# Kernel optimization log

Hardware: AMD Instinct MI355X
Metric: run time of the kernel (lower is better)

## Reference

```python
import jax, jax.numpy as jnp
import numpy as np
from jax.ops import segment_sum

N = 100000      # nodes
E = 1600000     # edges
G = 128         # graphs in batch
D = 128         # input (embedding) dim
H = 128         # hidden dim
WALK = 16       # random-walk length
PED = 16        # PE embed dim
L = 5           # GNN layers
OUT = 10        # classes
EPS = 1e-5      # batchnorm eps


def setup_inputs() -> dict:
    key = jax.random.key(0)
    ks = jax.random.split(key, 32)
    f = lambda k, shp: (jax.random.normal(k, shp, dtype=jnp.float32) * 0.05)
    inp = {
        'x': jnp.zeros((N,), dtype=jnp.int64) if jax.config.jax_enable_x64 else jnp.zeros((N,), dtype=jnp.int32),
        'edge_index': jax.random.randint(ks[0], (2, E), 0, N),
        'batch': jnp.sort(jax.random.randint(ks[1], (N,), 0, G)),
        'emb_table': f(ks[2], (1, D)),
        'pe_w': f(ks[3], (WALK, PED)), 'pe_b': f(ks[4], (PED,)),
        'proj_w': f(ks[5], (D + PED, H)), 'proj_b': f(ks[6], (H,)),
        'gin_w1': f(ks[7], (L, H, H)), 'gin_b1': f(ks[8], (L, H)),
        'gin_w2': f(ks[9], (L, H, H)), 'gin_b2': f(ks[10], (L, H)),
        'bn_g': jnp.ones((L, H), jnp.float32), 'bn_b': jnp.zeros((L, H), jnp.float32),
        'ffn_w1': f(ks[11], (L, H, 2 * H)), 'ffn_b1': f(ks[12], (L, 2 * H)),
        'ffn_w2': f(ks[13], (L, 2 * H, H)), 'ffn_b2': f(ks[14], (L, H)),
        'ffn_bn_g': jnp.ones((L, H), jnp.float32), 'ffn_bn_b': jnp.zeros((L, H), jnp.float32),
        'out_w1': f(ks[15], (H, H)), 'out_b1': f(ks[16], (H,)),
        'out_w2': f(ks[17], (H, OUT)), 'out_b2': f(ks[18], (OUT,)),
    }
    return inp


def _batchnorm(h, g, b):
    # BatchNorm1d forward with batch statistics (training-mode math)
    mu = jnp.mean(h, axis=0)
    var = jnp.var(h, axis=0)
    return (h - mu) * jax.lax.rsqrt(var + EPS) * g + b


def _forward(emb_table, pe_w, pe_b, proj_w, proj_b, gin_w1, gin_b1, gin_w2, gin_b2,
             bn_g, bn_b, ffn_w1, ffn_b1, ffn_w2, ffn_b2, ffn_bn_g, ffn_bn_b,
             out_w1, out_b1, out_w2, out_b2, x, edge_index, batch):
    h0 = emb_table[x]                                # [N, D] (all indices are 0)

    # ---- RandomWalkPositionalEncoding (vectorized scatter-add per step) ----
    row0, col0 = edge_index[0], edge_index[1]
    loops = jnp.arange(N)
    row = jnp.concatenate([row0, loops])
    col = jnp.concatenate([col0, loops])             # self loops appended
    deg = segment_sum(jnp.ones(row.shape, jnp.float32), col, num_segments=N)
    dinv = jnp.where(deg > 0, jax.lax.rsqrt(jnp.maximum(deg, 1.0)), 0.0)
    norm_e = dinv[row] * dinv[col]                   # [E+N]

    cnt = segment_sum(jnp.ones((N,), jnp.float32), batch, num_segments=G)
    prob = 1.0 / jnp.maximum(cnt, 1.0)[batch]        # per-graph uniform init

    def rw_step(p, _):
        new_p = segment_sum(p[row] * norm_e, col, num_segments=N)
        return new_p * 0.9 + p * 0.1, p

    _, rw = jax.lax.scan(rw_step, prob, None, length=WALK)   # [WALK, N]
    pe = rw.T @ pe_w + pe_b                          # [N, PED]

    # ---- input projection ----
    h = jnp.concatenate([h0, pe], axis=-1) @ proj_w + proj_b # [N, H]

    # ---- stacked GIN layers with BN, residual and FFN (dropout = eval identity) ----
    for i in range(L):
        res = h
        agg = segment_sum(h[row0], col0, num_segments=N) + h  # GIN: (1+eps)x + sum_j x_j, eps=0
        z = jax.nn.relu(agg @ gin_w1[i] + gin_b1[i]) @ gin_w2[i] + gin_b2[i]
        z = jax.nn.relu(_batchnorm(z, bn_g[i], bn_b[i]))
        h = z + res
        res2 = h
        f = jax.nn.relu(h @ ffn_w1[i] + ffn_b1[i]) @ ffn_w2[i] + ffn_b2[i]
        h = _batchnorm(f + res2, ffn_bn_g[i], ffn_bn_b[i])

    # ---- global mean pooling + MLP head ----
    gsum = segment_sum(h, batch, num_segments=G)
    g = gsum / jnp.maximum(cnt, 1.0)[:, None]        # [G, H]
    out = jax.nn.relu(g @ out_w1 + out_b1) @ out_w2 + out_b2
    return out                                        # [G, OUT]


def reference(x, edge_index, batch, emb_table, pe_w, pe_b, proj_w, proj_b,
              gin_w1, gin_b1, gin_w2, gin_b2, bn_g, bn_b, ffn_w1, ffn_b1,
              ffn_w2, ffn_b2, ffn_bn_g, ffn_bn_b, out_w1, out_b1, out_w2, out_b2):
    return _forward(emb_table, pe_w, pe_b, proj_w, proj_b, gin_w1, gin_b1, gin_w2,
                    gin_b2, bn_g, bn_b, ffn_w1, ffn_b1, ffn_w2, ffn_b2,
                    ffn_bn_g, ffn_bn_b, out_w1, out_b1, out_w2, out_b2,
                    x, edge_index, batch)
```

## Files before the change

### kernel.cpp

```cpp
#include <hip/hip_runtime.h>
#include <math.h>

#define NN 100000
#define NE 1600000
#define NG 128
#define HD 128
#define WLK 16
#define NL 5
#define NOUT 10
#define BNEPS 1e-5f
#define CDIV(a,b) (((a)+(b)-1)/(b))

#define NBKT 782
#define NEB 400
#define EPB 4000
#define NSCAN (NBKT*NEB)
#define NSB CDIV(NSCAN,1024)
#define NBM 782

typedef float f32x4 __attribute__((ext_vector_type(4)));
typedef _Float16 f16x8 __attribute__((ext_vector_type(8)));
typedef unsigned short ushort_t;
typedef unsigned int uint_t;

__device__ __forceinline__ ushort_t f2h(float x) {
    union { _Float16 h; ushort_t u; } c;
    c.h = (_Float16)x;
    return c.u;
}
__device__ __forceinline__ float h2f(ushort_t u) {
    union { ushort_t u; _Float16 h; } c;
    c.u = u;
    return (float)c.h;
}

__global__ void k_cnt(const int* __restrict__ batch, int* __restrict__ cnt,
                      int* __restrict__ goff) {
    int g = threadIdx.x;
    if (g >= NG) return;
    int lo0 = 0, hi0 = NN;
    while (lo0 < hi0) { int m = (lo0 + hi0) >> 1; if (batch[m] < g) lo0 = m + 1; else hi0 = m; }
    int lo1 = lo0, hi1 = NN;
    while (lo1 < hi1) { int m = (lo1 + hi1) >> 1; if (batch[m] < g + 1) lo1 = m + 1; else hi1 = m; }
    cnt[g] = lo1 - lo0;
    goff[g] = lo0;
}

__global__ void k_bhist(const int* __restrict__ col0, int* __restrict__ bhist) {
    __shared__ int hist[NBKT];
    for (int i = threadIdx.x; i < NBKT; i += 256) hist[i] = 0;
    __syncthreads();
    int e0 = blockIdx.x * EPB;
    for (int e = e0 + threadIdx.x; e < e0 + EPB; e += 256) atomicAdd(&hist[col0[e] >> 7], 1);
    __syncthreads();
    for (int i = threadIdx.x; i < NBKT; i += 256) bhist[i * NEB + blockIdx.x] = hist[i];
}

__global__ void k_gscan1(const int* __restrict__ in, int* __restrict__ bsum) {
    __shared__ int sm[256];
    int base = blockIdx.x * 1024 + threadIdx.x * 4;
    int s = 0;
#pragma unroll
    for (int i = 0; i < 4; ++i) { int e = base + i; if (e < NSCAN) s += in[e]; }
    sm[threadIdx.x] = s; __syncthreads();
    for (int st = 128; st > 0; st >>= 1) {
        if (threadIdx.x < st) sm[threadIdx.x] += sm[threadIdx.x + st];
        __syncthreads();
    }
    if (threadIdx.x == 0) bsum[blockIdx.x] = sm[0];
}

__global__ void k_scan2(int* __restrict__ blksum, int nblk) {
    __shared__ int sm[512];
    int t = threadIdx.x;
    int x = (t < nblk) ? blksum[t] : 0;
    sm[t] = x; __syncthreads();
    for (int s = 1; s < 512; s <<= 1) {
        int v = (t >= s) ? sm[t - s] : 0;
        __syncthreads();
        sm[t] += v;
        __syncthreads();
    }
    if (t < nblk) blksum[t] = sm[t] - x;
}

__global__ void k_gscan3(const int* __restrict__ in, const int* __restrict__ bsum,
                         int* __restrict__ out) {
    __shared__ int sm[256];
    int t = threadIdx.x;
    int base = blockIdx.x * 1024 + t * 4;
    int v[4]; int s = 0;
#pragma unroll
    for (int i = 0; i < 4; ++i) { int e = base + i; v[i] = (e < NSCAN) ? in[e] : 0; s += v[i]; }
    sm[t] = s; __syncthreads();
    for (int st = 1; st < 256; st <<= 1) {
        int x = (t >= st) ? sm[t - st] : 0;
        __syncthreads();
        sm[t] += x;
        __syncthreads();
    }
    int excl = sm[t] - s + bsum[blockIdx.x];
#pragma unroll
    for (int i = 0; i < 4; ++i) { int e = base + i; if (e < NSCAN) { out[e] = excl; excl += v[i]; } }
}

__global__ void k_escatter(const int* __restrict__ row0, const int* __restrict__ col0,
                           const int* __restrict__ boffs, int2* __restrict__ epair) {
    __shared__ int cur[NBKT];
    for (int i = threadIdx.x; i < NBKT; i += 256) cur[i] = boffs[i * NEB + blockIdx.x];
    __syncthreads();
    int e0 = blockIdx.x * EPB;
    for (int e = e0 + threadIdx.x; e < e0 + EPB; e += 256) {
        int c = col0[e], r = row0[e];
        int pos = atomicAdd(&cur[c >> 7], 1);
        epair[pos] = make_int2(c, r);
    }
}

__global__ void k_bucket(const int2* __restrict__ epair, const int* __restrict__ boffs,
                         int* __restrict__ rowptr, int* __restrict__ deg,
                         int* __restrict__ esrc) {
    __shared__ int cnt_[128], scn[128], cur_[128];
    int bkt = blockIdx.x, t = threadIdx.x;
    int bs = boffs[bkt * NEB];
    int be = (bkt + 1 < NBKT) ? boffs[(bkt + 1) * NEB] : NE;
    if (t < 128) cnt_[t] = 0;
    __syncthreads();
    for (int e = bs + t; e < be; e += 256) atomicAdd(&cnt_[epair[e].x & 127], 1);
    __syncthreads();
    int c = (t < 128) ? cnt_[t] : 0;
    if (t < 128) scn[t] = c;
    __syncthreads();
    for (int st = 1; st < 128; st <<= 1) {
        int x = (t >= st && t < 128) ? scn[t - st] : 0;
        __syncthreads();
        if (t < 128) scn[t] += x;
        __syncthreads();
    }
    if (t < 128) {
        int excl = scn[t] - c;
        int node = bkt * 128 + t;
        if (node < NN) { rowptr[node] = bs + excl; deg[node] = c; }
        cur_[t] = bs + excl;
    }
    if (bkt == NBKT - 1 && t == 0) rowptr[NN] = NE;
    __syncthreads();
    for (int e = bs + t; e < be; e += 256) {
        int2 p = epair[e];
        int pos = atomicAdd(&cur_[p.x & 127], 1);
        esrc[pos] = p.y;
    }
}

__global__ void k_init_pe(const int* __restrict__ deg, const int* __restrict__ batch,
                          const int* __restrict__ cnt, float* __restrict__ dinv,
                          float* __restrict__ p, float* __restrict__ pd) {
    int v = blockIdx.x * 256 + threadIdx.x;
    if (v >= NN) return;
    float dv = rsqrtf((float)(deg[v] + 1));
    dinv[v] = dv;
    float pv = 1.0f / fmaxf((float)cnt[batch[v]], 1.0f);
    p[v] = pv; pd[v] = pv * dv;
}

__global__ void k_rw_step(const float* __restrict__ pin, const float* __restrict__ pdin,
                          const int* __restrict__ rowptr, const int* __restrict__ esrc,
                          const float* __restrict__ dinv, float* __restrict__ rwslice,
                          float* __restrict__ pout, float* __restrict__ pdout) {
    int v = blockIdx.x * 256 + threadIdx.x;
    if (v >= NN) return;
    int b = rowptr[v], e = rowptr[v + 1];
    float a0 = 0.f, a1 = 0.f, a2 = 0.f, a3 = 0.f;
    int i = b;
    for (; i + 4 <= e; i += 4) {
        int s0 = esrc[i], s1 = esrc[i + 1], s2 = esrc[i + 2], s3 = esrc[i + 3];
        a0 += pdin[s0]; a1 += pdin[s1]; a2 += pdin[s2]; a3 += pdin[s3];
    }
    for (; i < e; ++i) a0 += pdin[esrc[i]];
    float s = (a0 + a1) + (a2 + a3);
    float dv = dinv[v];
    float pv = pin[v];
    float np = s * dv + pv * dv * dv;
    float nxt = 0.9f * np + 0.1f * pv;
    rwslice[v] = pv;
    pout[v] = nxt;
    pdout[v] = nxt * dv;
}

__global__ void k_mc1(const float* __restrict__ emb, const float* __restrict__ pe_w,
                      const float* __restrict__ pe_b, const float* __restrict__ proj_w,
                      const float* __restrict__ proj_b, float* __restrict__ M,
                      float* __restrict__ c1) {
    int j = threadIdx.x;
    float c0 = proj_b[j];
    for (int d = 0; d < HD; ++d) c0 += emb[d] * proj_w[d * HD + j];
    for (int w = 0; w < WLK; ++w) c0 += pe_b[w] * proj_w[(HD + w) * HD + j];
    c1[j] = c0;
    for (int s = 0; s < WLK; ++s) {
        float m = 0.f;
        for (int w = 0; w < WLK; ++w) m += pe_w[s * WLK + w] * proj_w[(HD + w) * HD + j];
        M[s * HD + j] = m;
    }
}

__global__ void k_proj(const float* __restrict__ rw, const float* __restrict__ M,
                       const float* __restrict__ c1, float4* __restrict__ h4,
                       uint2* __restrict__ hb4) {
    int idx = blockIdx.x * 256 + threadIdx.x;
    if (idx >= NN * 32) return;
    int v = idx >> 5, cg = (idx & 31) * 4;
    float4 acc = *(const float4*)&c1[cg];
#pragma unroll
    for (int s = 0; s < WLK; ++s) {
        float r = rw[s * NN + v];
        float4 m = *(const float4*)&M[s * HD + cg];
        acc.x += r * m.x; acc.y += r * m.y; acc.z += r * m.z; acc.w += r * m.w;
    }
    h4[idx] = acc;
    hb4[idx] = make_uint2((uint_t)f2h(acc.x) | ((uint_t)f2h(acc.y) << 16),
                          (uint_t)f2h(acc.z) | ((uint_t)f2h(acc.w) << 16));
}

__global__ void k_prepw(const float* __restrict__ g1, const float* __restrict__ g2,
                        const float* __restrict__ f1, const float* __restrict__ f2,
                        ushort_t* __restrict__ wt1, ushort_t* __restrict__ wt2,
                        ushort_t* __restrict__ wt3, ushort_t* __restrict__ wt4) {
    int i = blockIdx.x * 256 + threadIdx.x;
    if (i < 81920) {
        int l = i >> 14, rem = i & 16383, n = rem >> 7, k = rem & 127;
        wt1[i] = f2h(g1[l * 16384 + k * 128 + n]);
    } else if (i < 163840) {
        int j = i - 81920;
        int l = j >> 14, rem = j & 16383, n = rem >> 7, k = rem & 127;
        wt2[j] = f2h(g2[l * 16384 + k * 128 + n]);
    } else if (i < 327680) {
        int j = i - 163840;
        int l = j >> 15, rem = j & 32767, n = rem >> 7, k = rem & 127;
        wt3[j] = f2h(f1[l * 32768 + k * 256 + n]);
    } else {
        int j = i - 327680;
        int l = j >> 15, rem = j & 32767, n = rem >> 8, k = rem & 255;
        wt4[j] = f2h(f2[l * 32768 + k * 128 + n]);
    }
}

__global__ void k_aggb(const uint_t* __restrict__ hb2, const int* __restrict__ rowptr,
                       const int* __restrict__ esrc, uint_t* __restrict__ aggb2) {
    int wave = threadIdx.x >> 6, lane = threadIdx.x & 63;
    int v = blockIdx.x * 4 + wave;
    if (v >= NN) return;
    uint_t u = hb2[(size_t)v * 64 + lane];
    float sx[8], sy[8];
#pragma unroll
    for (int k = 0; k < 8; ++k) { sx[k] = 0.f; sy[k] = 0.f; }
    sx[0] = h2f((ushort_t)(u & 0xFFFFu)); sy[0] = h2f((ushort_t)(u >> 16));
    int b = rowptr[v], e = rowptr[v + 1];
    int i = b;
    for (; i + 8 <= e; i += 8) {
        int idx[8]; uint_t x[8];
#pragma unroll
        for (int k = 0; k < 8; ++k) idx[k] = esrc[i + k];
#pragma unroll
        for (int k = 0; k < 8; ++k) x[k] = hb2[(size_t)idx[k] * 64 + lane];
#pragma unroll
        for (int k = 0; k < 8; ++k) {
            sx[k] += h2f((ushort_t)(x[k] & 0xFFFFu));
            sy[k] += h2f((ushort_t)(x[k] >> 16));
        }
    }
    for (; i < e; ++i) {
        uint_t x = hb2[(size_t)esrc[i] * 64 + lane];
        sx[0] += h2f((ushort_t)(x & 0xFFFFu)); sy[0] += h2f((ushort_t)(x >> 16));
    }
    float fx = ((sx[0] + sx[1]) + (sx[2] + sx[3])) + ((sx[4] + sx[5]) + (sx[6] + sx[7]));
    float fy = ((sy[0] + sy[1]) + (sy[2] + sy[3])) + ((sy[4] + sy[5]) + (sy[6] + sy[7]));
    aggb2[(size_t)v * 64 + lane] = (uint_t)f2h(fx) | ((uint_t)f2h(fy) << 16);
}

#define GLDK 136
__global__ __launch_bounds__(256)
void k_gin(const ushort_t* __restrict__ A, const ushort_t* __restrict__ W1T,
           const ushort_t* __restrict__ W2T, const float* __restrict__ b1,
           const float* __restrict__ b2, ushort_t* __restrict__ z2h,
           float* __restrict__ partS, float* __restrict__ partQ) {
    __shared__ ushort_t As[128 * GLDK];
    __shared__ ushort_t Ws[64 * GLDK];
    __shared__ float sS[128], sQ[128];
    const int tid = threadIdx.x;
    const int w = tid >> 6, l = tid & 63;
    const int lm = l & 15, lq = l >> 4;
    const int rw0 = w * 32;
    const int vr0 = blockIdx.x * 128;
    if (tid < 128) { sS[tid] = 0.f; sQ[tid] = 0.f; }

#pragma unroll
    for (int it = 0; it < 8; ++it) {
        int f = it * 256 + tid;
        int row = f >> 4, sl = f & 15;
        uint4 a = make_uint4(0, 0, 0, 0);
        int vr = vr0 + row;
        if (vr < NN) a = *(const uint4*)&A[(size_t)vr * HD + sl * 8];
        *(uint4*)&As[row * GLDK + sl * 8] = a;
    }

    f32x4 z1a[2][2][4] = {};
    for (int c = 0; c < 2; ++c) {
        __syncthreads();
#pragma unroll
        for (int it = 0; it < 4; ++it) {
            int f = it * 256 + tid;
            int row = f >> 4, sl = f & 15;
            *(uint4*)&Ws[row * GLDK + sl * 8] =
                *(const uint4*)&W1T[(size_t)(c * 64 + row) * HD + sl * 8];
        }
        __syncthreads();
#pragma unroll
        for (int kk = 0; kk < 128; kk += 32) {
            f16x8 af[2], bf[4];
#pragma unroll
            for (int i = 0; i < 2; ++i)
                af[i] = *(const f16x8*)&As[(rw0 + i * 16 + lm) * GLDK + kk + lq * 8];
#pragma unroll
            for (int j = 0; j < 4; ++j)
                bf[j] = *(const f16x8*)&Ws[(j * 16 + lm) * GLDK + kk + lq * 8];
#pragma unroll
            for (int i = 0; i < 2; ++i)
#pragma unroll
                for (int j = 0; j < 4; ++j)
                    z1a[c][i][j] = __builtin_amdgcn_mfma_f32_16x16x32_f16(af[i], bf[j], z1a[c][i][j], 0, 0, 0);
        }
    }
    __syncthreads();

#pragma unroll
    for (int c = 0; c < 2; ++c)
#pragma unroll
        for (int j = 0; j < 4; ++j) {
            int col = c * 64 + j * 16 + lm;
            float bj = b1[col];
#pragma unroll
            for (int i = 0; i < 2; ++i)
#pragma unroll
                for (int r = 0; r < 4; ++r) {
                    int row = rw0 + i * 16 + lq * 4 + r;
                    As[row * GLDK + col] = f2h(fmaxf(z1a[c][i][j][r] + bj, 0.f));
                }
        }

    f32x4 z2a[2][2][4] = {};
    for (int c2 = 0; c2 < 2; ++c2) {
        __syncthreads();
#pragma unroll
        for (int it = 0; it < 4; ++it) {
            int f = it * 256 + tid;
            int row = f >> 4, sl = f & 15;
            *(uint4*)&Ws[row * GLDK + sl * 8] =
                *(const uint4*)&W2T[(size_t)(c2 * 64 + row) * HD + sl * 8];
        }
        __syncthreads();
#pragma unroll
        for (int kk = 0; kk < 128; kk += 32) {
            f16x8 af[2], bf[4];
#pragma unroll
            for (int i = 0; i < 2; ++i)
                af[i] = *(const f16x8*)&As[(rw0 + i * 16 + lm) * GLDK + kk + lq * 8];
#pragma unroll
            for (int j = 0; j < 4; ++j)
                bf[j] = *(const f16x8*)&Ws[(j * 16 + lm) * GLDK + kk + lq * 8];
#pragma unroll
            for (int i = 0; i < 2; ++i)
#pragma unroll
                for (int j = 0; j < 4; ++j)
                    z2a[c2][i][j] = __builtin_amdgcn_mfma_f32_16x16x32_f16(af[i], bf[j], z2a[c2][i][j], 0, 0, 0);
        }
    }

    float ls[2][4] = {}, lsq[2][4] = {};
#pragma unroll
    for (int c2 = 0; c2 < 2; ++c2)
#pragma unroll
        for (int j = 0; j < 4; ++j) {
            int col = c2 * 64 + j * 16 + lm;
            float bj = b2[col];
#pragma unroll
            for (int i = 0; i < 2; ++i)
#pragma unroll
                for (int r = 0; r < 4; ++r) {
                    int vr = vr0 + rw0 + i * 16 + lq * 4 + r;
                    if (vr < NN) {
                        float x = z2a[c2][i][j][r] + bj;
                        ls[c2][j] += x; lsq[c2][j] += x * x;
                        z2h[(size_t)vr * HD + col] = f2h(x);
                    }
                }
        }
#pragma unroll
    for (int c2 = 0; c2 < 2; ++c2)
#pragma unroll
        for (int j = 0; j < 4; ++j) {
            atomicAdd(&sS[c2 * 64 + j * 16 + lm], ls[c2][j]);
            atomicAdd(&sQ[c2 * 64 + j * 16 + lm], lsq[c2][j]);
        }
    __syncthreads();
    if (tid < 128) {
        partS[(size_t)tid * NBM + blockIdx.x] = sS[tid];
        partQ[(size_t)tid * NBM + blockIdx.x] = sQ[tid];
    }
}

template <int K, bool RELU, bool OUTH16, bool ADDRES, bool DOSTATS>
__global__ __launch_bounds__(256, 2)
void k_mgemm(const ushort_t* __restrict__ A, const ushort_t* __restrict__ WT,
             const float* __restrict__ bias, ushort_t* __restrict__ Ch,
             float* __restrict__ Cf, const float* __restrict__ res,
             float* __restrict__ partS, float* __restrict__ partQ, int ncols) {
    constexpr int LDK = 72;
    __shared__ ushort_t As[128 * LDK];
    __shared__ ushort_t Ws[128 * LDK];
    __shared__ float sS[128], sQ[128];
    const int tid = threadIdx.x;
    const int w = tid >> 6, l = tid & 63;
    const int lm = l & 15, lq = l >> 4;
    const int rb = (w >> 1) * 64, cbw = (w & 1) * 64;
    const int vr0 = blockIdx.x * 128;
    const int cb = blockIdx.y * 128;
    f32x4 acc[4][4] = {};

    for (int kt = 0; kt < K / 64; ++kt) {
        __syncthreads();
#pragma unroll
        for (int it = 0; it < 4; ++it) {
            int f = it * 256 + tid;
            int row = f >> 3, sl = f & 7;
            uint4 a = make_uint4(0, 0, 0, 0);
            int vr = vr0 + row;
            if (vr < NN) a = *(const uint4*)&A[(size_t)vr * K + kt * 64 + sl * 8];
            *(uint4*)&As[row * LDK + sl * 8] = a;
            uint4 wv = *(const uint4*)&WT[(size_t)(cb + row) * K + kt * 64 + sl * 8];
            *(uint4*)&Ws[row * LDK + sl * 8] = wv;
        }
        __syncthreads();
#pragma unroll
        for (int kk = 0; kk < 64; kk += 32) {
            f16x8 af[4], bf[4];
#pragma unroll
            for (int i = 0; i < 4; ++i)
                af[i] = *(const f16x8*)&As[(rb + i * 16 + lm) * LDK + kk + lq * 8];
#pragma unroll
            for (int j = 0; j < 4; ++j)
                bf[j] = *(const f16x8*)&Ws[(cbw + j * 16 + lm) * LDK + kk + lq * 8];
#pragma unroll
            for (int i = 0; i < 4; ++i)
#pragma unroll
                for (int j = 0; j < 4; ++j)
                    acc[i][j] = __builtin_amdgcn_mfma_f32_16x16x32_f16(af[i], bf[j], acc[i][j], 0, 0, 0);
        }
    }

    float bcol[4];
#pragma unroll
    for (int j = 0; j < 4; ++j) bcol[j] = bias[cb + cbw + j * 16 + lm];
    if (DOSTATS && tid < 128) { sS[tid] = 0.f; sQ[tid] = 0.f; }
    __syncthreads();
    float ls[4] = {0, 0, 0, 0}, lsq[4] = {0, 0, 0, 0};
#pragma unroll
    for (int i = 0; i < 4; ++i) {
#pragma unroll
        for (int r = 0; r < 4; ++r) {
            int vr = vr0 + rb + i * 16 + lq * 4 + r;
            if (vr < NN) {
#pragma unroll
                for (int j = 0; j < 4; ++j) {
                    float x = acc[i][j][r] + bcol[j];
                    if (RELU) x = fmaxf(x, 0.f);
                    int c = cb + cbw + j * 16 + lm;
                    if (ADDRES) x += res[(size_t)vr * ncols + c];
                    if (DOSTATS) { ls[j] += x; lsq[j] += x * x; }
                    if (OUTH16) Ch[(size_t)vr * ncols + c] = f2h(x);
                    else        Cf[(size_t)vr * ncols + c] = x;
                }
            }
        }
    }
    if (DOSTATS) {
#pragma unroll
        for (int j = 0; j < 4; ++j) {
            atomicAdd(&sS[cbw + j * 16 + lm], ls[j]);
            atomicAdd(&sQ[cbw + j * 16 + lm], lsq[j]);
        }
        __syncthreads();
        if (tid < 128) {
            partS[(size_t)(cb + tid) * NBM + blockIdx.x] = sS[tid];
            partQ[(size_t)(cb + tid) * NBM + blockIdx.x] = sQ[tid];
        }
    }
}

__global__ void k_bnparm(const float* __restrict__ partS, const float* __restrict__ partQ,
                         const float* __restrict__ g, const float* __restrict__ b,
                         float* __restrict__ bnA, float* __restrict__ bnB) {
    __shared__ float smS[256], smQ[256];
    int c = blockIdx.x, t = threadIdx.x;
    float s = 0.f, q = 0.f;
    for (int i = t; i < NBM; i += 256) {
        s += partS[(size_t)c * NBM + i];
        q += partQ[(size_t)c * NBM + i];
    }
    smS[t] = s; smQ[t] = q; __syncthreads();
    for (int st = 128; st > 0; st >>= 1) {
        if (t < st) { smS[t] += smS[t + st]; smQ[t] += smQ[t + st]; }
        __syncthreads();
    }
    if (t == 0) {
        float mu = smS[0] * (1.0f / NN);
        float var = smQ[0] * (1.0f / NN) - mu * mu;
        float inv = rsqrtf(var + BNEPS);
        float a = g[c] * inv;
        bnA[c] = a;
        bnB[c] = b[c] - mu * a;
    }
}

__global__ void k_bn_relu_res(const uint2* __restrict__ z4, const float* __restrict__ bnA,
                              const float* __restrict__ bnB, float4* __restrict__ h4,
                              uint2* __restrict__ hb4) {
    int idx = blockIdx.x * 256 + threadIdx.x;
    if (idx >= NN * 32) return;
    int cg = (idx & 31) * 4;
    float4 A = *(const float4*)&bnA[cg];
    float4 B = *(const float4*)&bnB[cg];
    uint2 zv = z4[idx];
    float z0 = h2f((ushort_t)(zv.x & 0xFFFFu)), z1 = h2f((ushort_t)(zv.x >> 16));
    float z2 = h2f((ushort_t)(zv.y & 0xFFFFu)), z3 = h2f((ushort_t)(zv.y >> 16));
    float4 hv = h4[idx];
    float4 nh;
    nh.x = hv.x + fmaxf(z0 * A.x + B.x, 0.f);
    nh.y = hv.y + fmaxf(z1 * A.y + B.y, 0.f);
    nh.z = hv.z + fmaxf(z2 * A.z + B.z, 0.f);
    nh.w = hv.w + fmaxf(z3 * A.w + B.w, 0.f);
    h4[idx] = nh;
    hb4[idx] = make_uint2((uint_t)f2h(nh.x) | ((uint_t)f2h(nh.y) << 16),
                          (uint_t)f2h(nh.z) | ((uint_t)f2h(nh.w) << 16));
}

__global__ void k_bn(const uint2* __restrict__ t4, const float* __restrict__ bnA,
                     const float* __restrict__ bnB, float4* __restrict__ h4,
                     uint2* __restrict__ hb4) {
    int idx = blockIdx.x * 256 + threadIdx.x;
    if (idx >= NN * 32) return;
    int cg = (idx & 31) * 4;
    float4 A = *(const float4*)&bnA[cg];
    float4 B = *(const float4*)&bnB[cg];
    uint2 tv = t4[idx];
    float t0 = h2f((ushort_t)(tv.x & 0xFFFFu)), t1 = h2f((ushort_t)(tv.x >> 16));
    float t2 = h2f((ushort_t)(tv.y & 0xFFFFu)), t3 = h2f((ushort_t)(tv.y >> 16));
    float4 nh;
    nh.x = t0 * A.x + B.x;
    nh.y = t1 * A.y + B.y;
    nh.z = t2 * A.z + B.z;
    nh.w = t3 * A.w + B.w;
    h4[idx] = nh;
    hb4[idx] = make_uint2((uint_t)f2h(nh.x) | ((uint_t)f2h(nh.y) << 16),
                          (uint_t)f2h(nh.z) | ((uint_t)f2h(nh.w) << 16));
}

__global__ void k_pool(const float4* __restrict__ h4, const int* __restrict__ goff,
                       const int* __restrict__ cnt, float* __restrict__ gsum) {
    __shared__ float4 sm[256];
    int g = blockIdx.x >> 2, sub = blockIdx.x & 3;
    int n0 = goff[g], n = cnt[g];
    int cg = threadIdx.x & 31, rl = threadIdx.x >> 5;
    float4 acc = make_float4(0.f, 0.f, 0.f, 0.f);
    for (int r = sub * 8 + rl; r < n; r += 32) {
        float4 v = h4[(size_t)(n0 + r) * 32 + cg];
        acc.x += v.x; acc.y += v.y; acc.z += v.z; acc.w += v.w;
    }
    sm[threadIdx.x] = acc; __syncthreads();
    for (int st = 128; st >= 32; st >>= 1) {
        if (threadIdx.x < st) {
            float4 o = sm[threadIdx.x + st];
            sm[threadIdx.x].x += o.x; sm[threadIdx.x].y += o.y;
            sm[threadIdx.x].z += o.z; sm[threadIdx.x].w += o.w;
        }
        __syncthreads();
    }
    if (threadIdx.x < 32) {
        float4 v = sm[threadIdx.x];
        atomicAdd(&gsum[g * HD + cg * 4 + 0], v.x);
        atomicAdd(&gsum[g * HD + cg * 4 + 1], v.y);
        atomicAdd(&gsum[g * HD + cg * 4 + 2], v.z);
        atomicAdd(&gsum[g * HD + cg * 4 + 3], v.w);
    }
}

__global__ void k_head(const float* __restrict__ gsum, const int* __restrict__ cnt,
                       const float* __restrict__ w1, const float* __restrict__ b1,
                       const float* __restrict__ w2, const float* __restrict__ b2,
                       float* __restrict__ out) {
    __shared__ float gv[HD], av[HD];
    int gid = blockIdx.x, t = threadIdx.x;
    float c = fmaxf((float)cnt[gid], 1.0f);
    gv[t] = gsum[gid * HD + t] / c;
    __syncthreads();
    float a = b1[t];
    for (int k = 0; k < HD; ++k) a += gv[k] * w1[k * HD + t];
    av[t] = fmaxf(a, 0.f);
    __syncthreads();
    if (t < NOUT) {
        float o = b2[t];
        for (int k = 0; k < HD; ++k) o += av[k] * w2[k * NOUT + t];
        out[gid * NOUT + t] = o;
    }
}

static constexpr size_t AL(size_t x) { return (x + 511) & ~(size_t)511; }
static constexpr size_t OFF_H      = 0;
static constexpr size_t OFF_HB     = OFF_H      + AL((size_t)NN * HD * 4);
static constexpr size_t OFF_BUFF   = OFF_HB     + AL((size_t)NN * HD * 2);
static constexpr size_t OFF_SHARE  = OFF_BUFF   + AL((size_t)NN * HD * 4);
static constexpr size_t SZ_SHARE   = AL((size_t)NN * 256 * 2);
static constexpr size_t OFF_RW     = OFF_SHARE  + SZ_SHARE;
static constexpr size_t OFF_P0     = OFF_RW     + AL((size_t)WLK * NN * 4);
static constexpr size_t OFF_P1     = OFF_P0     + AL((size_t)NN * 4);
static constexpr size_t OFF_PD0    = OFF_P1     + AL((size_t)NN * 4);
static constexpr size_t OFF_PD1    = OFF_PD0    + AL((size_t)NN * 4);
static constexpr size_t OFF_DINV   = OFF_PD1    + AL((size_t)NN * 4);
static constexpr size_t OFF_ESRC   = OFF_DINV   + AL((size_t)NN * 4);
static constexpr size_t OFF_ROWPTR = OFF_ESRC   + AL((size_t)NE * 4);
static constexpr size_t OFF_DEG    = OFF_ROWPTR + AL((size_t)(NN + 1) * 4);
static constexpr size_t OFF_BHIST  = OFF_DEG    + AL((size_t)NN * 4);
static constexpr size_t OFF_BOFFS  = OFF_BHIST  + AL((size_t)NSCAN * 4);
static constexpr size_t OFF_BSUM   = OFF_BOFFS  + AL((size_t)NSCAN * 4);
static constexpr size_t OFF_WT1    = OFF_BSUM   + AL(512 * 4);
static constexpr size_t OFF_WT2    = OFF_WT1    + AL((size_t)5 * 16384 * 2);
static constexpr size_t OFF_WT3    = OFF_WT2    + AL((size_t)5 * 16384 * 2);
static constexpr size_t OFF_WT4    = OFF_WT3    + AL((size_t)5 * 32768 * 2);
static constexpr size_t OFF_PARTS  = OFF_WT4    + AL((size_t)5 * 32768 * 2);
static constexpr size_t OFF_PARTQ  = OFF_PARTS  + AL((size_t)128 * NBM * 4);
static constexpr size_t OFF_BNA    = OFF_PARTQ  + AL((size_t)128 * NBM * 4);
static constexpr size_t OFF_BNB    = OFF_BNA    + AL(128 * 4);
static constexpr size_t OFF_M      = OFF_BNB    + AL(128 * 4);
static constexpr size_t OFF_C1     = OFF_M      + AL((size_t)WLK * HD * 4);
static constexpr size_t OFF_CNT    = OFF_C1     + AL(HD * 4);
static constexpr size_t OFF_GOFF   = OFF_CNT    + AL(NG * 4);
static constexpr size_t OFF_GSUM   = OFF_GOFF   + AL(NG * 4);
static constexpr size_t ZERO_BYTES = (size_t)NG * HD * 4;

extern "C" void kernel_launch(void* const* d_in, const int* in_sizes, int n_in,
                              void* d_out, int out_size, void* d_ws, size_t ws_size,
                              hipStream_t stream) {
    const int* eidx = (const int*)d_in[1];
    const int* row0 = eidx;
    const int* col0 = eidx + NE;
    const int* batch = (const int*)d_in[2];
    const float* emb = (const float*)d_in[3];
    const float* pe_w = (const float*)d_in[4];
    const float* pe_b = (const float*)d_in[5];
    const float* proj_w = (const float*)d_in[6];
    const float* proj_b = (const float*)d_in[7];
    const float* gin_w1 = (const float*)d_in[8];
    const float* gin_b1 = (const float*)d_in[9];
    const float* gin_w2 = (const float*)d_in[10];
    const float* gin_b2 = (const float*)d_in[11];
    const float* bn_g = (const float*)d_in[12];
    const float* bn_b = (const float*)d_in[13];
    const float* ffn_w1 = (const float*)d_in[14];
    const float* ffn_b1 = (const float*)d_in[15];
    const float* ffn_w2 = (const float*)d_in[16];
    const float* ffn_b2 = (const float*)d_in[17];
    const float* ffn_bn_g = (const float*)d_in[18];
    const float* ffn_bn_b = (const float*)d_in[19];
    const float* out_w1 = (const float*)d_in[20];
    const float* out_b1 = (const float*)d_in[21];
    const float* out_w2 = (const float*)d_in[22];
    const float* out_b2 = (const float*)d_in[23];
    float* out = (float*)d_out;

    char* ws = (char*)d_ws;
    float*    h     = (float*)(ws + OFF_H);
    ushort_t* hb    = (ushort_t*)(ws + OFF_HB);
    ushort_t* th    = (ushort_t*)(ws + OFF_BUFF);
    ushort_t* aggh  = (ushort_t*)(ws + OFF_SHARE);
    ushort_t* z2h   = (ushort_t*)(ws + OFF_SHARE + (size_t)NN * HD * 2);
    ushort_t* f1h   = (ushort_t*)(ws + OFF_SHARE);
    int2*     epair = (int2*)(ws + OFF_SHARE);
    float*    rw    = (float*)(ws + OFF_RW);
    float*    p0    = (float*)(ws + OFF_P0);
    float*    p1    = (float*)(ws + OFF_P1);
    float*    pd0   = (float*)(ws + OFF_PD0);
    float*    pd1   = (float*)(ws + OFF_PD1);
    float*    dinv  = (float*)(ws + OFF_DINV);
    int*      esrc  = (int*)(ws + OFF_ESRC);
    int*      rowptr= (int*)(ws + OFF_ROWPTR);
    int*      deg   = (int*)(ws + OFF_DEG);
    int*      bhist = (int*)(ws + OFF_BHIST);
    int*      boffs = (int*)(ws + OFF_BOFFS);
    int*      bsum  = (int*)(ws + OFF_BSUM);
    ushort_t* wt1   = (ushort_t*)(ws + OFF_WT1);
    ushort_t* wt2   = (ushort_t*)(ws + OFF_WT2);
    ushort_t* wt3   = (ushort_t*)(ws + OFF_WT3);
    ushort_t* wt4   = (ushort_t*)(ws + OFF_WT4);
    float*    partS = (float*)(ws + OFF_PARTS);
    float*    partQ = (float*)(ws + OFF_PARTQ);
    float*    bnA   = (float*)(ws + OFF_BNA);
    float*    bnB   = (float*)(ws + OFF_BNB);
    float*    M     = (float*)(ws + OFF_M);
    float*    c1    = (float*)(ws + OFF_C1);
    int*      cnt   = (int*)(ws + OFF_CNT);
    int*      goff  = (int*)(ws + OFF_GOFF);
    float*    gsum  = (float*)(ws + OFF_GSUM);

    const int NB = CDIV(NN, 256);
    const int NBV = CDIV(NN * 32, 256);

    hipMemsetAsync(ws + OFF_GSUM, 0, ZERO_BYTES, stream);

    k_cnt<<<1, 128, 0, stream>>>(batch, cnt, goff);
    k_bhist<<<NEB, 256, 0, stream>>>(col0, bhist);
    k_gscan1<<<NSB, 256, 0, stream>>>(bhist, bsum);
    k_scan2<<<1, 512, 0, stream>>>(bsum, NSB);
    k_gscan3<<<NSB, 256, 0, stream>>>(bhist, bsum, boffs);
    k_escatter<<<NEB, 256, 0, stream>>>(row0, col0, boffs, epair);
    k_bucket<<<NBKT, 256, 0, stream>>>(epair, boffs, rowptr, deg, esrc);

    k_init_pe<<<NB, 256, 0, stream>>>(deg, batch, cnt, dinv, p0, pd0);
    k_mc1<<<1, 128, 0, stream>>>(emb, pe_w, pe_b, proj_w, proj_b, M, c1);
    k_prepw<<<1920, 256, 0, stream>>>(gin_w1, gin_w2, ffn_w1, ffn_w2, wt1, wt2, wt3, wt4);
    for (int s = 0; s < WLK; ++s) {
        const float* pin = (s & 1) ? p1 : p0;
        const float* pdin = (s & 1) ? pd1 : pd0;
        float* pout = (s & 1) ? p0 : p1;
        float* pdout = (s & 1) ? pd0 : pd1;
        k_rw_step<<<NB, 256, 0, stream>>>(pin, pdin, rowptr, esrc, dinv,
                                          rw + (size_t)s * NN, pout, pdout);
    }
    k_proj<<<NBV, 256, 0, stream>>>(rw, M, c1, (float4*)h, (uint2*)hb);

    dim3 g1(NBM, 1), g2(NBM, 2);
    for (int i = 0; i < NL; ++i) {
        k_aggb<<<CDIV(NN, 4), 256, 0, stream>>>((const uint_t*)hb, rowptr, esrc, (uint_t*)aggh);
        k_gin<<<NBM, 256, 0, stream>>>(aggh, wt1 + (size_t)i * 16384, wt2 + (size_t)i * 16384,
                                       gin_b1 + i * HD, gin_b2 + i * HD, z2h, partS, partQ);
        k_bnparm<<<128, 256, 0, stream>>>(partS, partQ, bn_g + i * HD, bn_b + i * HD, bnA, bnB);
        k_bn_relu_res<<<NBV, 256, 0, stream>>>(
            (const uint2*)z2h, bnA, bnB, (float4*)h, (uint2*)hb);
        k_mgemm<128, true, true, false, false><<<g2, 256, 0, stream>>>(
            hb, wt3 + (size_t)i * 32768, ffn_b1 + i * 256, f1h, nullptr, nullptr,
            nullptr, nullptr, 256);
        k_mgemm<256, false, true, true, true><<<g1, 256, 0, stream>>>(
            f1h, wt4 + (size_t)i * 32768, ffn_b2 + i * HD, th, nullptr, h,
            partS, partQ, 128);
        k_bnparm<<<128, 256, 0, stream>>>(partS, partQ, ffn_bn_g + i * HD, ffn_bn_b + i * HD, bnA, bnB);
        k_bn<<<NBV, 256, 0, stream>>>(
            (const uint2*)th, bnA, bnB, (float4*)h, (uint2*)hb);
    }

    k_pool<<<NG * 4, 256, 0, stream>>>((const float4*)h, goff, cnt, gsum);
    k_head<<<NG, 128, 0, stream>>>(gsum, cnt, out_w1, out_b1, out_w2, out_b2, out);
}
```

Measured before the change: 1.620 ms.

## Defer batchnorm application into consumers and fuse BN-residual into first FFN GEMM

Removes the standalone elementwise BN kernels. The post-FFN batchnorm affine is now applied lazily, folded into the aggregation epilogue as A*sum + deg*B, into the new ffn1 prologue, and into the head after pooling. The GIN BN+ReLU+residual is fused into the A-tile load of a new FFN1 GEMM kernel, which also writes the fp32 pre-FFN hidden state used as the residual. Only a half-precision pre-BN tensor is kept between layers, which cuts full-size fp32 read/write passes per layer. The trade-off is that the residual and aggregation now work on fp16 pre-normalization values, which may shift numerics.

```diff
diff --git a/kernel.cpp b/kernel.cpp
--- a/kernel.cpp
+++ b/kernel.cpp
@@ -190,8 +190,10 @@
 __global__ void k_mc1(const float* __restrict__ emb, const float* __restrict__ pe_w,
                       const float* __restrict__ pe_b, const float* __restrict__ proj_w,
                       const float* __restrict__ proj_b, float* __restrict__ M,
-                      float* __restrict__ c1) {
+                      float* __restrict__ c1, float* __restrict__ bnA0,
+                      float* __restrict__ bnB0) {
     int j = threadIdx.x;
+    bnA0[j] = 1.f; bnB0[j] = 0.f;
     float c0 = proj_b[j];
     for (int d = 0; d < HD; ++d) c0 += emb[d] * proj_w[d * HD + j];
     for (int w = 0; w < WLK; ++w) c0 += pe_b[w] * proj_w[(HD + w) * HD + j];
@@ -204,8 +206,7 @@
 }
 
 __global__ void k_proj(const float* __restrict__ rw, const float* __restrict__ M,
-                       const float* __restrict__ c1, float4* __restrict__ h4,
-                       uint2* __restrict__ hb4) {
+                       const float* __restrict__ c1, uint2* __restrict__ th4) {
     int idx = blockIdx.x * 256 + threadIdx.x;
     if (idx >= NN * 32) return;
     int v = idx >> 5, cg = (idx & 31) * 4;
@@ -216,8 +217,7 @@
         float4 m = *(const float4*)&M[s * HD + cg];
         acc.x += r * m.x; acc.y += r * m.y; acc.z += r * m.z; acc.w += r * m.w;
     }
-    h4[idx] = acc;
-    hb4[idx] = make_uint2((uint_t)f2h(acc.x) | ((uint_t)f2h(acc.y) << 16),
+    th4[idx] = make_uint2((uint_t)f2h(acc.x) | ((uint_t)f2h(acc.y) << 16),
                           (uint_t)f2h(acc.z) | ((uint_t)f2h(acc.w) << 16));
 }
 
@@ -244,12 +244,13 @@
     }
 }
 
-__global__ void k_aggb(const uint_t* __restrict__ hb2, const int* __restrict__ rowptr,
-                       const int* __restrict__ esrc, uint_t* __restrict__ aggb2) {
+__global__ void k_aggb(const uint_t* __restrict__ th2, const int* __restrict__ rowptr,
+                       const int* __restrict__ esrc, const float* __restrict__ bnA0,
+                       const float* __restrict__ bnB0, uint_t* __restrict__ aggb2) {
     int wave = threadIdx.x >> 6, lane = threadIdx.x & 63;
     int v = blockIdx.x * 4 + wave;
     if (v >= NN) return;
-    uint_t u = hb2[(size_t)v * 64 + lane];
+    uint_t u = th2[(size_t)v * 64 + lane];
     float sx[8], sy[8];
 #pragma unroll
     for (int k = 0; k < 8; ++k) { sx[k] = 0.f; sy[k] = 0.f; }
@@ -261,7 +262,7 @@
 #pragma unroll
         for (int k = 0; k < 8; ++k) idx[k] = esrc[i + k];
 #pragma unroll
-        for (int k = 0; k < 8; ++k) x[k] = hb2[(size_t)idx[k] * 64 + lane];
+        for (int k = 0; k < 8; ++k) x[k] = th2[(size_t)idx[k] * 64 + lane];
 #pragma unroll
         for (int k = 0; k < 8; ++k) {
             sx[k] += h2f((ushort_t)(x[k] & 0xFFFFu));
@@ -269,12 +270,17 @@
         }
     }
     for (; i < e; ++i) {
-        uint_t x = hb2[(size_t)esrc[i] * 64 + lane];
+        uint_t x = th2[(size_t)esrc[i] * 64 + lane];
         sx[0] += h2f((ushort_t)(x & 0xFFFFu)); sy[0] += h2f((ushort_t)(x >> 16));
     }
     float fx = ((sx[0] + sx[1]) + (sx[2] + sx[3])) + ((sx[4] + sx[5]) + (sx[6] + sx[7]));
     float fy = ((sy[0] + sy[1]) + (sy[2] + sy[3])) + ((sy[4] + sy[5]) + (sy[6] + sy[7]));
-    aggb2[(size_t)v * 64 + lane] = (uint_t)f2h(fx) | ((uint_t)f2h(fy) << 16);
+    float2 A = *(const float2*)&bnA0[lane * 2];
+    float2 B = *(const float2*)&bnB0[lane * 2];
+    float cf = (float)(e - b + 1);
+    float ox = A.x * fx + cf * B.x;
+    float oy = A.y * fy + cf * B.y;
+    aggb2[(size_t)v * 64 + lane] = (uint_t)f2h(ox) | ((uint_t)f2h(oy) << 16);
 }
 
 #define GLDK 136
@@ -405,6 +411,101 @@
     if (tid < 128) {
         partS[(size_t)tid * NBM + blockIdx.x] = sS[tid];
         partQ[(size_t)tid * NBM + blockIdx.x] = sQ[tid];
+    }
+}
+
+__global__ __launch_bounds__(256)
+void k_ffn1(const ushort_t* __restrict__ th, const ushort_t* __restrict__ z2h,
+            const ushort_t* __restrict__ W3T, const float* __restrict__ b3,
+            const float* __restrict__ bnA0, const float* __restrict__ bnB0,
+            const float* __restrict__ bnA1, const float* __restrict__ bnB1,
+            float* __restrict__ hmid, ushort_t* __restrict__ f1h) {
+    __shared__ ushort_t As[128 * GLDK];
+    __shared__ ushort_t Ws[64 * GLDK];
+    __shared__ float sA0[128], sB0[128], sA1[128], sB1[128];
+    const int tid = threadIdx.x;
+    const int w = tid >> 6, l = tid & 63;
+    const int lm = l & 15, lq = l >> 4;
+    const int rw0 = w * 32;
+    const int vr0 = blockIdx.x * 128;
+
+    if (tid < 128) {
+        sA0[tid] = bnA0[tid]; sB0[tid] = bnB0[tid];
+        sA1[tid] = bnA1[tid]; sB1[tid] = bnB1[tid];
+    }
+    __syncthreads();
+
+#pragma unroll
+    for (int it = 0; it < 8; ++it) {
+        int f = it * 256 + tid;
+        int row = f >> 4, sl = f & 15;
+        int vr = vr0 + row;
+        uint4 o = make_uint4(0, 0, 0, 0);
+        if (vr < NN) {
+            uint4 tv = *(const uint4*)&th[(size_t)vr * HD + sl * 8];
+            uint4 zv = *(const uint4*)&z2h[(size_t)vr * HD + sl * 8];
+            uint_t tu[4] = {tv.x, tv.y, tv.z, tv.w};
+            uint_t zu[4] = {zv.x, zv.y, zv.z, zv.w};
+            float hm[8];
+            uint_t ou[4];
+#pragma unroll
+            for (int m = 0; m < 4; ++m) {
+                int ch0 = sl * 8 + m * 2;
+                float t0 = h2f((ushort_t)(tu[m] & 0xFFFFu));
+                float t1 = h2f((ushort_t)(tu[m] >> 16));
+                float z0 = h2f((ushort_t)(zu[m] & 0xFFFFu));
+                float z1 = h2f((ushort_t)(zu[m] >> 16));
+                float h0 = sA0[ch0] * t0 + sB0[ch0] + fmaxf(sA1[ch0] * z0 + sB1[ch0], 0.f);
+                float h1 = sA0[ch0 + 1] * t1 + sB0[ch0 + 1] + fmaxf(sA1[ch0 + 1] * z1 + sB1[ch0 + 1], 0.f);
+                hm[m * 2] = h0; hm[m * 2 + 1] = h1;
+                ou[m] = (uint_t)f2h(h0) | ((uint_t)f2h(h1) << 16);
+            }
+            o = make_uint4(ou[0], ou[1], ou[2], ou[3]);
+            *(float4*)&hmid[(size_t)vr * HD + sl * 8] = make_float4(hm[0], hm[1], hm[2], hm[3]);
+            *(float4*)&hmid[(size_t)vr * HD + sl * 8 + 4] = make_float4(hm[4], hm[5], hm[6], hm[7]);
+        }
+        *(uint4*)&As[row * GLDK + sl * 8] = o;
+    }
+
+    for (int c = 0; c < 4; ++c) {
+        __syncthreads();
+#pragma unroll
+        for (int it = 0; it < 4; ++it) {
+            int f = it * 256 + tid;
+            int row = f >> 4, sl = f & 15;
+            *(uint4*)&Ws[row * GLDK + sl * 8] =
+                *(const uint4*)&W3T[(size_t)(c * 64 + row) * HD + sl * 8];
+        }
+        __syncthreads();
+        f32x4 acc[2][4] = {};
+#pragma unroll
+        for (int kk = 0; kk < 128; kk += 32) {
+            f16x8 af[2], bf[4];
+#pragma unroll
+            for (int i = 0; i < 2; ++i)
+                af[i] = *(const f16x8*)&As[(rw0 + i * 16 + lm) * GLDK + kk + lq * 8];
+#pragma unroll
+            for (int j = 0; j < 4; ++j)
+                bf[j] = *(const f16x8*)&Ws[(j * 16 + lm) * GLDK + kk + lq * 8];
+#pragma unroll
+            for (int i = 0; i < 2; ++i)
+#pragma unroll
+                for (int j = 0; j < 4; ++j)
+                    acc[i][j] = __builtin_amdgcn_mfma_f32_16x16x32_f16(af[i], bf[j], acc[i][j], 0, 0, 0);
+        }
+#pragma unroll
+        for (int j = 0; j < 4; ++j) {
+            int col = c * 64 + j * 16 + lm;
+            float bj = b3[col];
+#pragma unroll
+            for (int i = 0; i < 2; ++i)
+#pragma unroll
+                for (int r = 0; r < 4; ++r) {
+                    int vr = vr0 + rw0 + i * 16 + lq * 4 + r;
+                    if (vr < NN)
+                        f1h[(size_t)vr * 256 + col] = f2h(fmaxf(acc[i][j][r] + bj, 0.f));
+                }
+        }
     }
 }
 
@@ -521,50 +622,7 @@
     }
 }
 
-__global__ void k_bn_relu_res(const uint2* __restrict__ z4, const float* __restrict__ bnA,
-                              const float* __restrict__ bnB, float4* __restrict__ h4,
-                              uint2* __restrict__ hb4) {
-    int idx = blockIdx.x * 256 + threadIdx.x;
-    if (idx >= NN * 32) return;
-    int cg = (idx & 31) * 4;
-    float4 A = *(const float4*)&bnA[cg];
-    float4 B = *(const float4*)&bnB[cg];
-    uint2 zv = z4[idx];
-    float z0 = h2f((ushort_t)(zv.x & 0xFFFFu)), z1 = h2f((ushort_t)(zv.x >> 16));
-    float z2 = h2f((ushort_t)(zv.y & 0xFFFFu)), z3 = h2f((ushort_t)(zv.y >> 16));
-    float4 hv = h4[idx];
-    float4 nh;
-    nh.x = hv.x + fmaxf(z0 * A.x + B.x, 0.f);
-    nh.y = hv.y + fmaxf(z1 * A.y + B.y, 0.f);
-    nh.z = hv.z + fmaxf(z2 * A.z + B.z, 0.f);
-    nh.w = hv.w + fmaxf(z3 * A.w + B.w, 0.f);
-    h4[idx] = nh;
-    hb4[idx] = make_uint2((uint_t)f2h(nh.x) | ((uint_t)f2h(nh.y) << 16),
-                          (uint_t)f2h(nh.z) | ((uint_t)f2h(nh.w) << 16));
-}
-
-__global__ void k_bn(const uint2* __restrict__ t4, const float* __restrict__ bnA,
-                     const float* __restrict__ bnB, float4* __restrict__ h4,
-                     uint2* __restrict__ hb4) {
-    int idx = blockIdx.x * 256 + threadIdx.x;
-    if (idx >= NN * 32) return;
-    int cg = (idx & 31) * 4;
-    float4 A = *(const float4*)&bnA[cg];
-    float4 B = *(const float4*)&bnB[cg];
-    uint2 tv = t4[idx];
-    float t0 = h2f((ushort_t)(tv.x & 0xFFFFu)), t1 = h2f((ushort_t)(tv.x >> 16));
-    float t2 = h2f((ushort_t)(tv.y & 0xFFFFu)), t3 = h2f((ushort_t)(tv.y >> 16));
-    float4 nh;
-    nh.x = t0 * A.x + B.x;
-    nh.y = t1 * A.y + B.y;
-    nh.z = t2 * A.z + B.z;
-    nh.w = t3 * A.w + B.w;
-    h4[idx] = nh;
-    hb4[idx] = make_uint2((uint_t)f2h(nh.x) | ((uint_t)f2h(nh.y) << 16),
-                          (uint_t)f2h(nh.z) | ((uint_t)f2h(nh.w) << 16));
-}
-
-__global__ void k_pool(const float4* __restrict__ h4, const int* __restrict__ goff,
+__global__ void k_pool(const uint2* __restrict__ th4, const int* __restrict__ goff,
                        const int* __restrict__ cnt, float* __restrict__ gsum) {
     __shared__ float4 sm[256];
     int g = blockIdx.x >> 2, sub = blockIdx.x & 3;
@@ -572,8 +630,11 @@
     int cg = threadIdx.x & 31, rl = threadIdx.x >> 5;
     float4 acc = make_float4(0.f, 0.f, 0.f, 0.f);
     for (int r = sub * 8 + rl; r < n; r += 32) {
-        float4 v = h4[(size_t)(n0 + r) * 32 + cg];
-        acc.x += v.x; acc.y += v.y; acc.z += v.z; acc.w += v.w;
+        uint2 v = th4[(size_t)(n0 + r) * 32 + cg];
+        acc.x += h2f((ushort_t)(v.x & 0xFFFFu));
+        acc.y += h2f((ushort_t)(v.x >> 16));
+        acc.z += h2f((ushort_t)(v.y & 0xFFFFu));
+        acc.w += h2f((ushort_t)(v.y >> 16));
     }
     sm[threadIdx.x] = acc; __syncthreads();
     for (int st = 128; st >= 32; st >>= 1) {
@@ -594,13 +655,14 @@
 }
 
 __global__ void k_head(const float* __restrict__ gsum, const int* __restrict__ cnt,
+                       const float* __restrict__ bnA0, const float* __restrict__ bnB0,
                        const float* __restrict__ w1, const float* __restrict__ b1,
                        const float* __restrict__ w2, const float* __restrict__ b2,
                        float* __restrict__ out) {
     __shared__ float gv[HD], av[HD];
     int gid = blockIdx.x, t = threadIdx.x;
     float c = fmaxf((float)cnt[gid], 1.0f);
-    gv[t] = gsum[gid * HD + t] / c;
+    gv[t] = bnA0[t] * (gsum[gid * HD + t] / c) + bnB0[t];
     __syncthreads();
     float a = b1[t];
     for (int k = 0; k < HD; ++k) a += gv[k] * w1[k * HD + t];
@@ -614,12 +676,12 @@
 }
 
 static constexpr size_t AL(size_t x) { return (x + 511) & ~(size_t)511; }
-static constexpr size_t OFF_H      = 0;
-static constexpr size_t OFF_HB     = OFF_H      + AL((size_t)NN * HD * 4);
-static constexpr size_t OFF_BUFF   = OFF_HB     + AL((size_t)NN * HD * 2);
-static constexpr size_t OFF_SHARE  = OFF_BUFF   + AL((size_t)NN * HD * 4);
+static constexpr size_t OFF_HMID   = 0;
+static constexpr size_t OFF_TH     = OFF_HMID   + AL((size_t)NN * HD * 4);
+static constexpr size_t OFF_SHARE  = OFF_TH     + AL((size_t)NN * HD * 2);
 static constexpr size_t SZ_SHARE   = AL((size_t)NN * 256 * 2);
-static constexpr size_t OFF_RW     = OFF_SHARE  + SZ_SHARE;
+static constexpr size_t OFF_Z2     = OFF_SHARE  + SZ_SHARE;
+static constexpr size_t OFF_RW     = OFF_Z2     + AL((size_t)NN * HD * 2);
 static constexpr size_t OFF_P0     = OFF_RW     + AL((size_t)WLK * NN * 4);
 static constexpr size_t OFF_P1     = OFF_P0     + AL((size_t)NN * 4);
 static constexpr size_t OFF_PD0    = OFF_P1     + AL((size_t)NN * 4);
@@ -637,9 +699,11 @@
 static constexpr size_t OFF_WT4    = OFF_WT3    + AL((size_t)5 * 32768 * 2);
 static constexpr size_t OFF_PARTS  = OFF_WT4    + AL((size_t)5 * 32768 * 2);
 static constexpr size_t OFF_PARTQ  = OFF_PARTS  + AL((size_t)128 * NBM * 4);
-static constexpr size_t OFF_BNA    = OFF_PARTQ  + AL((size_t)128 * NBM * 4);
-static constexpr size_t OFF_BNB    = OFF_BNA    + AL(128 * 4);
-static constexpr size_t OFF_M      = OFF_BNB    + AL(128 * 4);
+static constexpr size_t OFF_BNA0   = OFF_PARTQ  + AL((size_t)128 * NBM * 4);
+static constexpr size_t OFF_BNB0   = OFF_BNA0   + AL(128 * 4);
+static constexpr size_t OFF_BNA1   = OFF_BNB0   + AL(128 * 4);
+static constexpr size_t OFF_BNB1   = OFF_BNA1   + AL(128 * 4);
+static constexpr size_t OFF_M      = OFF_BNB1   + AL(128 * 4);
 static constexpr size_t OFF_C1     = OFF_M      + AL((size_t)WLK * HD * 4);
 static constexpr size_t OFF_CNT    = OFF_C1     + AL(HD * 4);
 static constexpr size_t OFF_GOFF   = OFF_CNT    + AL(NG * 4);
@@ -677,12 +741,11 @@
     float* out = (float*)d_out;
 
     char* ws = (char*)d_ws;
-    float*    h     = (float*)(ws + OFF_H);
-    ushort_t* hb    = (ushort_t*)(ws + OFF_HB);
-    ushort_t* th    = (ushort_t*)(ws + OFF_BUFF);
+    float*    hmid  = (float*)(ws + OFF_HMID);
+    ushort_t* th    = (ushort_t*)(ws + OFF_TH);
     ushort_t* aggh  = (ushort_t*)(ws + OFF_SHARE);
-    ushort_t* z2h   = (ushort_t*)(ws + OFF_SHARE + (size_t)NN * HD * 2);
     ushort_t* f1h   = (ushort_t*)(ws + OFF_SHARE);
+    ushort_t* z2h   = (ushort_t*)(ws + OFF_Z2);
     int2*     epair = (int2*)(ws + OFF_SHARE);
     float*    rw    = (float*)(ws + OFF_RW);
     float*    p0    = (float*)(ws + OFF_P0);
@@ -702,8 +765,10 @@
     ushort_t* wt4   = (ushort_t*)(ws + OFF_WT4);
     float*    partS = (float*)(ws + OFF_PARTS);
     float*    partQ = (float*)(ws + OFF_PARTQ);
-    float*    bnA   = (float*)(ws + OFF_BNA);
-    float*    bnB   = (float*)(ws + OFF_BNB);
+    float*    bnA0  = (float*)(ws + OFF_BNA0);
+    float*    bnB0  = (float*)(ws + OFF_BNB0);
+    float*    bnA1  = (float*)(ws + OFF_BNA1);
+    float*    bnB1  = (float*)(ws + OFF_BNB1);
     float*    M     = (float*)(ws + OFF_M);
     float*    c1    = (float*)(ws + OFF_C1);
     int*      cnt   = (int*)(ws + OFF_CNT);
@@ -724,7 +789,7 @@
     k_bucket<<<NBKT, 256, 0, stream>>>(epair, boffs, rowptr, deg, esrc);
 
     k_init_pe<<<NB, 256, 0, stream>>>(deg, batch, cnt, dinv, p0, pd0);
-    k_mc1<<<1, 128, 0, stream>>>(emb, pe_w, pe_b, proj_w, proj_b, M, c1);
+    k_mc1<<<1, 128, 0, stream>>>(emb, pe_w, pe_b, proj_w, proj_b, M, c1, bnA0, bnB0);
     k_prepw<<<1920, 256, 0, stream>>>(gin_w1, gin_w2, ffn_w1, ffn_w2, wt1, wt2, wt3, wt4);
     for (int s = 0; s < WLK; ++s) {
         const float* pin = (s & 1) ? p1 : p0;
@@ -734,27 +799,24 @@
         k_rw_step<<<NB, 256, 0, stream>>>(pin, pdin, rowptr, esrc, dinv,
                                           rw + (size_t)s * NN, pout, pdout);
     }
-    k_proj<<<NBV, 256, 0, stream>>>(rw, M, c1, (float4*)h, (uint2*)hb);
-
-    dim3 g1(NBM, 1), g2(NBM, 2);
+    k_proj<<<NBV, 256, 0, stream>>>(rw, M, c1, (uint2*)th);
+
+    dim3 g1(NBM, 1);
     for (int i = 0; i < NL; ++i) {
-        k_aggb<<<CDIV(NN, 4), 256, 0, stream>>>((const uint_t*)hb, rowptr, esrc, (uint_t*)aggh);
+        k_aggb<<<CDIV(NN, 4), 256, 0, stream>>>((const uint_t*)th, rowptr, esrc,
+                                                bnA0, bnB0, (uint_t*)aggh);
         k_gin<<<NBM, 256, 0, stream>>>(aggh, wt1 + (size_t)i * 16384, wt2 + (size_t)i * 16384,
                                        gin_b1 + i * HD, gin_b2 + i * HD, z2h, partS, partQ);
-        k_bnparm<<<128, 256, 0, stream>>>(partS, partQ, bn_g + i * HD, bn_b + i * HD, bnA, bnB);
-        k_bn_relu_res<<<NBV, 256, 0, stream>>>(
-            (const uint2*)z2h, bnA, bnB, (float4*)h, (uint2*)hb);
-        k_mgemm<128, true, true, false, false><<<g2, 256, 0, stream>>>(
-            hb, wt3 + (size_t)i * 32768, ffn_b1 + i * 256, f1h, nullptr, nullptr,
-            nullptr, nullptr, 256);
+        k_bnparm<<<128, 256, 0, stream>>>(partS, partQ, bn_g + i * HD, bn_b + i * HD, bnA1, bnB1);
+        k_ffn1<<<NBM, 256, 0, stream>>>(th, z2h, wt3 + (size_t)i * 32768, ffn_b1 + i * 256,
+                                        bnA0, bnB0, bnA1, bnB1, hmid, f1h);
         k_mgemm<256, false, true, true, true><<<g1, 256, 0, stream>>>(
-            f1h, wt4 + (size_t)i * 32768, ffn_b2 + i * HD, th, nullptr, h,
+            f1h, wt4 + (size_t)i * 32768, ffn_b2 + i * HD, th, nullptr, hmid,
             partS, partQ, 128);
-        k_bnparm<<<128, 256, 0, stream>>>(partS, partQ, ffn_bn_g + i * HD, ffn_bn_b + i * HD, bnA, bnB);
-        k_bn<<<NBV, 256, 0, stream>>>(
-            (const uint2*)th, bnA, bnB, (float4*)h, (uint2*)hb);
-    }
-
-    k_pool<<<NG * 4, 256, 0, stream>>>((const float4*)h, goff, cnt, gsum);
-    k_head<<<NG, 128, 0, stream>>>(gsum, cnt, out_w1, out_b1, out_w2, out_b2, out);
-}
+        k_bnparm<<<128, 256, 0, stream>>>(partS, partQ, ffn_bn_g + i * HD, ffn_bn_b + i * HD,
+                                          bnA0, bnB0);
+    }
+
+    k_pool<<<NG * 4, 256, 0, stream>>>((const uint2*)th, goff, cnt, gsum);
+    k_head<<<NG, 128, 0, stream>>>(gsum, cnt, bnA0, bnB0, out_w1, out_b1, out_w2, out_b2, out);
+}
```

Result: faster. 1.585 ms (-2.2%).
